# Optimization experiments

Hardware: AMD Instinct MI355X
Metric: run time of the kernel (lower is better)

Reference implementation:

```python
import jax, jax.numpy as jnp
import numpy as np

DIM = 1152
N_HEADS = 12
GROUPS = 6
KV_HEADS = N_HEADS // GROUPS  # 2
HEAD_DIM = DIM // N_HEADS     # 96
BASE = 10000.0
BSZ = 4
SEQ = 2048
MAX_SEQ = 2048
NEG_INF = -1e9


def rope(x, start_pos):
    # x: [b, s, h, d]; interleaved (even/odd) rotary embedding, matching the torch code
    b, s, h, d = x.shape
    x_even = x[..., 0::2]
    x_odd = x[..., 1::2]
    # even positions <- -x_odd, odd positions <- x_even (interleaved)
    x_rev = jnp.stack([-x_odd, x_even], axis=-1).reshape(x.shape)
    i = jnp.repeat(jnp.arange(0, d, 2), 2).astype(x.dtype)  # [d]
    theta = 1.0 / (BASE ** (i / d))                          # [d]
    pos = jnp.arange(start_pos + s, dtype=x.dtype)           # [s] (start_pos=0 case, as in source)
    ang = pos[:, None] * theta[None, :]                      # [s, d]
    cos = jnp.cos(ang).reshape(1, s, 1, d)
    sin = jnp.sin(ang).reshape(1, s, 1, d)
    return x * cos + x_rev * sin


def setup_inputs() -> dict:
    key = jax.random.key(0)
    ks = jax.random.split(key, 4)
    sc = 0.02
    x = jax.random.normal(ks[0], (BSZ, SEQ, DIM), jnp.float32)
    # causal mask [S, end_pos]: 0 on/below diagonal, large negative above
    mask = jnp.triu(jnp.full((SEQ, SEQ), NEG_INF, jnp.float32), k=1)
    q_w = jax.random.normal(ks[1], (DIM, DIM), jnp.float32) * sc
    q_b = jnp.zeros((DIM,), jnp.float32)
    kv_w = jax.random.normal(ks[2], (2 * KV_HEADS * HEAD_DIM, DIM), jnp.float32) * sc
    kv_b = jnp.zeros((2 * KV_HEADS * HEAD_DIM,), jnp.float32)
    wo_w = jax.random.normal(ks[3], (DIM, DIM), jnp.float32) * sc
    wo_b = jnp.zeros((DIM,), jnp.float32)
    return {"x": x, "mask": mask, "q_w": q_w, "q_b": q_b, "kv_w": kv_w,
            "kv_b": kv_b, "wo_w": wo_w, "wo_b": wo_b, "start_pos": 0}


def reference(x, mask, q_w, q_b, kv_w, kv_b, wo_w, wo_b, start_pos):
    b, s, f = x.shape
    end = start_pos + s
    q = (x @ q_w.T + q_b).reshape(b, s, N_HEADS, HEAD_DIM)
    kv = (x @ kv_w.T + kv_b).reshape(b, s, 2, KV_HEADS, HEAD_DIM)
    k, v = kv[:, :, 0], kv[:, :, 1]
    rq = rope(q, start_pos)
    rk = rope(k, start_pos)
    # KV-cache write (cache initialized to zeros, as in the buffer)
    k_cache = jnp.zeros((b, MAX_SEQ, KV_HEADS, HEAD_DIM), x.dtype).at[:, start_pos:end].set(rk)
    v_cache = jnp.zeros((b, MAX_SEQ, KV_HEADS, HEAD_DIM), x.dtype).at[:, start_pos:end].set(v)
    # repeat_kv: head index = kv_head * groups + g  -> jnp.repeat along head axis
    kk = jnp.repeat(k_cache[:, :end], GROUPS, axis=2)  # [b, t, H, d]
    vv = jnp.repeat(v_cache[:, :end], GROUPS, axis=2)
    scale = HEAD_DIM ** -0.5
    attn = jnp.einsum('bshd,bthd->bsht', rq, kk) * scale
    attn = attn + mask[:, None, :]  # mask [s, t] -> [s, 1, t] broadcast over b, h
    scores = jax.nn.softmax(attn.astype(jnp.float32), axis=-1).astype(x.dtype)
    out = jnp.einsum('bsht,bthd->bshd', scores, vv).reshape(b, s, DIM)
    return out @ wo_w.T + wo_b
```

## Files before the change

### kernel.cpp

```cpp
#include <hip/hip_runtime.h>
#include <hip/hip_bf16.h>

constexpr int DIMD  = 1152;
constexpr int NHD   = 12;
constexpr int KVHD  = 2;
constexpr int HDD   = 96;
constexpr int GRPS  = 6;
constexpr int SEQL  = 2048;
constexpr int BSZ4  = 4;
constexpr int MROWS = BSZ4 * SEQL;
constexpr int NQKV  = DIMD + 2 * KVHD * HDD;
constexpr float SCALE = 0.10206207261596577f;

typedef short  bf16x8 __attribute__((ext_vector_type(8)));
typedef float  f32x4  __attribute__((ext_vector_type(4)));

typedef __attribute__((address_space(3))) unsigned int       lds_u32_t;
typedef __attribute__((address_space(1))) const unsigned int glb_u32_t;

__device__ __forceinline__ void gload16(const unsigned short* g, unsigned short* l) {
    __builtin_amdgcn_global_load_lds((glb_u32_t*)(const void*)g,
                                     (lds_u32_t*)(void*)l, 16, 0, 0);
}

__device__ __forceinline__ unsigned short f2bf(float f) {
    unsigned int u = __builtin_bit_cast(unsigned int, f);
    u += 0x7fff + ((u >> 16) & 1);
    return (unsigned short)(u >> 16);
}

__device__ __forceinline__ unsigned cvtpk(float a, float b) {
    unsigned r;
    asm volatile("v_cvt_pk_bf16_f32 %0, %1, %2" : "=v"(r) : "v"(a), "v"(b));
    return r;
}

__device__ __forceinline__ void cvt4(const float4* __restrict__ s,
                                     ushort4* __restrict__ d, int i) {
    float4 f = s[i];
    ushort4 o;
    o.x = f2bf(f.x); o.y = f2bf(f.y); o.z = f2bf(f.z); o.w = f2bf(f.w);
    d[i] = o;
}

__global__ __launch_bounds__(256) void prep_kernel(
    const float4* __restrict__ x,   const float4* __restrict__ qw,
    const float4* __restrict__ kvw, const float4* __restrict__ wow,
    ushort4* __restrict__ xb,   ushort4* __restrict__ qwb,
    ushort4* __restrict__ kvwb, ushort4* __restrict__ wowb,
    const int* __restrict__ sp, float2* __restrict__ tab)
{
    constexpr int X4  = MROWS * DIMD / 4;
    constexpr int W4  = DIMD * DIMD / 4;
    constexpr int KV4 = 2 * KVHD * HDD * DIMD/4;
    constexpr int NT  = SEQL * 48;
    int i = blockIdx.x * 256 + threadIdx.x;
    if (i < X4)  { cvt4(x, xb, i); return; }
    i -= X4;
    if (i < W4)  { cvt4(qw, qwb, i); return; }
    i -= W4;
    if (i < KV4) { cvt4(kvw, kvwb, i); return; }
    i -= KV4;
    if (i < W4)  { cvt4(wow, wowb, i); return; }
    i -= W4;
    if (i < NT) {
        int s = i / 48, j = i - (i / 48) * 48;
        float th = powf(10000.0f, -(float)(2 * j) / 96.0f);
        float ang = (float)(s + *sp) * th;
        float sn, cs; sincosf(ang, &sn, &cs);
        tab[i] = make_float2(cs, sn);
    }
}

__global__ __launch_bounds__(256) void qkv_mfma_kernel(
    const unsigned short* __restrict__ xb,  const unsigned short* __restrict__ qwb,
    const unsigned short* __restrict__ kvwb,
    const float* __restrict__ qb,  const float* __restrict__ kvb,
    const float2* __restrict__ tab,
    unsigned short* __restrict__ Qo, unsigned short* __restrict__ Ko,
    unsigned short* __restrict__ VTo)
{
    __shared__ __align__(16) unsigned short As[2][128 * 32];
    __shared__ __align__(16) unsigned short Bs[2][128 * 32];

    const int tid  = threadIdx.x;
    const int w    = tid >> 6;
    const int lane = tid & 63;
    const int l16  = lane & 15;
    const int quad = lane >> 4;
    const int wm   = w >> 1, wn = w & 1;
    const int m0   = blockIdx.y * 128;
    const int n0   = blockIdx.x * 128;

    const unsigned short* Abase = xb + (size_t)m0 * DIMD;
    const unsigned short* Bbase = (n0 < DIMD)
        ? qwb  + (size_t)n0 * DIMD
        : kvwb + (size_t)(n0 - DIMD) * DIMD;

    const int srow = w * 16 + (lane >> 2);
    const int scol = (lane & 3) * 8;

    f32x4 acc[4][4];
    #pragma unroll
    for (int mi = 0; mi < 4; mi++)
        #pragma unroll
        for (int ni = 0; ni < 4; ni++) acc[mi][ni] = (f32x4){0.f, 0.f, 0.f, 0.f};

    constexpr int NK = DIMD / 32;

    gload16(Abase + (size_t)srow        * DIMD + scol, &As[0][w * 512]);
    gload16(Abase + (size_t)(srow + 64) * DIMD + scol, &As[0][2048 + w * 512]);
    gload16(Bbase + (size_t)srow        * DIMD + scol, &Bs[0][w * 512]);
    gload16(Bbase + (size_t)(srow + 64) * DIMD + scol, &Bs[0][2048 + w * 512]);

    for (int kt = 0; kt < NK; kt++) {
        const int cur = kt & 1;
        if (kt + 1 < NK) {
            const int k0 = (kt + 1) * 32;
            gload16(Abase + (size_t)srow        * DIMD + k0 + scol, &As[cur ^ 1][w * 512]);
            gload16(Abase + (size_t)(srow + 64) * DIMD + k0 + scol, &As[cur ^ 1][2048 + w * 512]);
            gload16(Bbase + (size_t)srow        * DIMD + k0 + scol, &Bs[cur ^ 1][w * 512]);
            gload16(Bbase + (size_t)(srow + 64) * DIMD + k0 + scol, &Bs[cur ^ 1][2048 + w * 512]);
            asm volatile("s_waitcnt vmcnt(4)" ::: "memory");
        } else {
            asm volatile("s_waitcnt vmcnt(0)" ::: "memory");
        }
        __builtin_amdgcn_s_barrier();
        asm volatile("" ::: "memory");

        bf16x8 af[4], bfr[4];
        #pragma unroll
        for (int mi = 0; mi < 4; mi++)
            af[mi] = *(const bf16x8*)&As[cur][(wm * 64 + mi * 16 + l16) * 32 + quad * 8];
        #pragma unroll
        for (int ni = 0; ni < 4; ni++)
            bfr[ni] = *(const bf16x8*)&Bs[cur][(wn * 64 + ni * 16 + l16) * 32 + quad * 8];
        #pragma unroll
        for (int mi = 0; mi < 4; mi++)
            #pragma unroll
            for (int ni = 0; ni < 4; ni++)
                acc[mi][ni] = __builtin_amdgcn_mfma_f32_16x16x32_bf16(
                    af[mi], bfr[ni], acc[mi][ni], 0, 0, 0);

        asm volatile("" ::: "memory");
        __builtin_amdgcn_s_barrier();
    }

    #pragma unroll
    for (int ni = 0; ni < 4; ni++) {
        const int n   = n0 + wn * 64 + ni * 16 + l16;
        const bool isQ = (n < DIMD);
        const int jj  = n - DIMD;
        const bool isK = !isQ && (jj < KVHD * HDD);
        const int d   = isQ ? (n % HDD) : (jj % HDD);
        const int hh  = isQ ? (n / HDD) : ((jj / HDD) & 1);
        const float bias = isQ ? qb[n] : kvb[jj];
        const bool doRope = isQ || isK;
        const int de2 = (d >> 1);
        const float sg = (n & 1) ? 1.0f : -1.0f;
        #pragma unroll
        for (int mi = 0; mi < 4; mi++) {
            #pragma unroll
            for (int r = 0; r < 4; r++) {
                const int m = m0 + wm * 64 + mi * 16 + quad * 4 + r;
                const int b = m >> 11;
                const int s = m & (SEQL - 1);
                float v  = acc[mi][ni][r] + bias;
                float pv = __shfl_xor(v, 1, 64);
                float o = v;
                if (doRope) {
                    float2 cs2 = tab[s * 48 + de2];
                    o = v * cs2.x + sg * pv * cs2.y;
                }
                if (isQ)
                    Qo[(((size_t)b * NHD + hh) * SEQL + s) * HDD + d] = f2bf(o);
                else if (isK)
                    Ko[(((size_t)b * KVHD + hh) * SEQL + s) * HDD + d] = f2bf(o);
                else
                    VTo[(((size_t)b * KVHD + hh) * HDD + d) * SEQL + s] = f2bf(o);
            }
        }
    }
}

__global__ __launch_bounds__(256, 3) void attn_mfma_kernel(
    const unsigned short* __restrict__ Q, const unsigned short* __restrict__ K,
    const unsigned short* __restrict__ VT, unsigned short* __restrict__ AO)
{
    constexpr int KHALF = 64 * 104;
    __shared__ __align__(16) unsigned short Ks[2 * KHALF];
    __shared__ __align__(16) unsigned short VTs[96 * 72];
    __shared__ __align__(16) unsigned short Ps[4][16 * 72];
    __shared__ float Al[4][16];

    const int tid  = threadIdx.x;
    const int w    = tid >> 6;
    const int lane = tid & 63;
    const int l16  = lane & 15;
    const int quad = lane >> 4;

    const int idx = (int)blockIdx.x;
    const int qi  = idx / 48;
    const int hb  = idx - qi * 48;
    const int qt  = 31 - qi;
    const int h   = hb % NHD;
    const int b   = hb / NHD;
    const int kvh = h / GRPS;
    const int nkb = qt + 1;

    const unsigned short* Qbase  = Q  + (((size_t)b * NHD  + h)   * SEQL) * HDD;
    const unsigned short* Kbase  = K  + (((size_t)b * KVHD + kvh) * SEQL) * HDD;
    const unsigned short* VTbase = VT + (((size_t)b * KVHD + kvh) * HDD)  * SEQL;

    int goff[7]; int gkind[7]; int loff[7];
    #pragma unroll
    for (int j = 0; j < 7; j++) {
        const int i = w + 4 * j;
        gkind[j] = 2; goff[j] = 0; loff[j] = 0;
        if (i < 13) {
            int slot = i * 64 + lane;
            int r = slot / 13, g = slot - r * 13;
            goff[j]  = r * HDD + (g < 12 ? g * 8 : 0);
            gkind[j] = 0;
            loff[j]  = i * 512;
        } else if (i < 27) {
            int iv = i - 13;
            int slot = iv * 64 + lane;
            if (slot < 864) {
                int r = slot / 9, g = slot - r * 9;
                goff[j]  = r * SEQL + (g < 8 ? g * 8 : 0);
                gkind[j] = 1;
                loff[j]  = iv * 512;
            }
        }
    }

    bf16x8 qf[3];
    {
        const int qrow = qt * 64 + w * 16 + l16;
        const unsigned short* qp = Qbase + (size_t)qrow * HDD + quad * 8;
        qf[0] = *(const bf16x8*)(qp);
        qf[1] = *(const bf16x8*)(qp + 32);
        qf[2] = *(const bf16x8*)(qp + 64);
    }

    float m_r = -1e30f, l_r = 0.0f;
    f32x4 oacc[6];
    #pragma unroll
    for (int nn = 0; nn < 6; nn++) oacc[nn] = (f32x4){0.f, 0.f, 0.f, 0.f};

    #pragma unroll
    for (int j = 0; j < 7; j++)
        if (gkind[j] == 0)
            gload16(Kbase + goff[j], &Ks[loff[j]]);
    #pragma unroll
    for (int j = 0; j < 7; j++)
        if (gkind[j] == 1) {
            if ((w + 4 * j) < 26 || lane < 32)
                gload16(VTbase + goff[j], &VTs[loff[j]]);
        }

    const int dql = w * 16 + l16;

    for (int kb = 0; kb < nkb; kb++) {
        const int  cur  = kb & 1;
        const bool more = (kb + 1 < nkb);

        if (more) {
            const size_t kg = (size_t)(kb + 1) * 64 * HDD;
            #pragma unroll
            for (int j = 0; j < 7; j++)
                if (gkind[j] == 0)
                    gload16(Kbase + kg + goff[j], &Ks[(cur ^ 1) * KHALF + loff[j]]);
            asm volatile("s_waitcnt vmcnt(6)" ::: "memory");
        } else {
            asm volatile("s_waitcnt vmcnt(3)" ::: "memory");
        }
        __builtin_amdgcn_s_barrier();
        asm volatile("" ::: "memory");

        const unsigned short* ksb = &Ks[cur * KHALF];
        f32x4 s[4];
        __builtin_amdgcn_s_setprio(1);
        #pragma unroll
        for (int n = 0; n < 4; n++) {
            const unsigned short* kr = ksb + (n * 16 + l16) * 104 + quad * 8;
            bf16x8 kf0 = *(const bf16x8*)(kr);
            bf16x8 kf1 = *(const bf16x8*)(kr + 32);
            bf16x8 kf2 = *(const bf16x8*)(kr + 64);
            f32x4 a = (f32x4){0.f, 0.f, 0.f, 0.f};
            a = __builtin_amdgcn_mfma_f32_16x16x32_bf16(kf0, qf[0], a, 0, 0, 0);
            a = __builtin_amdgcn_mfma_f32_16x16x32_bf16(kf1, qf[1], a, 0, 0, 0);
            a = __builtin_amdgcn_mfma_f32_16x16x32_bf16(kf2, qf[2], a, 0, 0, 0);
            s[n] = a;
        }
        __builtin_amdgcn_s_setprio(0);

        float v[4][4];
        float mx = -3e30f;
        if (!more) {
            #pragma unroll
            for (int n = 0; n < 4; n++)
                #pragma unroll
                for (int r = 0; r < 4; r++) {
                    float x = s[n][r] * SCALE;
                    if (n * 16 + quad * 4 + r > dql) x = -1e30f;
                    v[n][r] = x;
                    mx = fmaxf(mx, x);
                }
        } else {
            #pragma unroll
            for (int n = 0; n < 4; n++)
                #pragma unroll
                for (int r = 0; r < 4; r++) {
                    float x = s[n][r] * SCALE;
                    v[n][r] = x;
                    mx = fmaxf(mx, x);
                }
        }
        mx = fmaxf(mx, __shfl_xor(mx, 16, 64));
        mx = fmaxf(mx, __shfl_xor(mx, 32, 64));
        const float mnew = fmaxf(m_r, mx);
        const float al = __expf(m_r - mnew);
        if (quad == 0) Al[w][l16] = al;
        float sum = 0.0f;
        #pragma unroll
        for (int n = 0; n < 4; n++) {
            float p0 = __expf(v[n][0] - mnew);
            float p1 = __expf(v[n][1] - mnew);
            float p2 = __expf(v[n][2] - mnew);
            float p3 = __expf(v[n][3] - mnew);
            sum += (p0 + p1) + (p2 + p3);
            uint2 pk;
            pk.x = cvtpk(p0, p1);
            pk.y = cvtpk(p2, p3);
            *(uint2*)&Ps[w][l16 * 72 + n * 16 + quad * 4] = pk;
        }
        sum += __shfl_xor(sum, 16, 64);
        sum += __shfl_xor(sum, 32, 64);
        l_r = l_r * al + sum;
        m_r = mnew;
        __builtin_amdgcn_wave_barrier();

        const float4 alb = *(const float4*)&Al[w][quad * 4];
        bf16x8 pa0 = *(const bf16x8*)&Ps[w][l16 * 72 + quad * 8];
        bf16x8 pa1 = *(const bf16x8*)&Ps[w][l16 * 72 + 32 + quad * 8];
        const float albr[4] = {alb.x, alb.y, alb.z, alb.w};

        if (more) asm volatile("s_waitcnt vmcnt(3)" ::: "memory");
        else      asm volatile("s_waitcnt vmcnt(0)" ::: "memory");
        __builtin_amdgcn_s_barrier();
        asm volatile("" ::: "memory");

        __builtin_amdgcn_s_setprio(1);
        #pragma unroll
        for (int nn = 0; nn < 6; nn++) {
            const unsigned short* vr = &VTs[(nn * 16 + l16) * 72 + quad * 8];
            bf16x8 vb0 = *(const bf16x8*)(vr);
            bf16x8 vb1 = *(const bf16x8*)(vr + 32);
            f32x4 a = oacc[nn];
            #pragma unroll
            for (int r = 0; r < 4; r++) a[r] *= albr[r];
            a = __builtin_amdgcn_mfma_f32_16x16x32_bf16(pa0, vb0, a, 0, 0, 0);
            a = __builtin_amdgcn_mfma_f32_16x16x32_bf16(pa1, vb1, a, 0, 0, 0);
            oacc[nn] = a;
        }
        __builtin_amdgcn_s_setprio(0);

        asm volatile("" ::: "memory");
        __builtin_amdgcn_s_barrier();
        asm volatile("" ::: "memory");

        if (more) {
            const int kg = (kb + 1) * 64;
            #pragma unroll
            for (int j = 0; j < 7; j++)
                if (gkind[j] == 1) {
                    if ((w + 4 * j) < 26 || lane < 32)
                        gload16(VTbase + kg + goff[j], &VTs[loff[j]]);
                }
        }
    }

    const float linv = 1.0f / l_r;
    if (quad == 0) Al[w][l16] = linv;
    __builtin_amdgcn_wave_barrier();
    const float4 lb4 = *(const float4*)&Al[w][quad * 4];
    const float lbr[4] = {lb4.x, lb4.y, lb4.z, lb4.w};
    const int row0 = qt * 64 + w * 16 + quad * 4;
    #pragma unroll
    for (int nn = 0; nn < 6; nn++) {
        #pragma unroll
        for (int r = 0; r < 4; r++) {
            AO[((size_t)b * SEQL + row0 + r) * DIMD + h * HDD + nn * 16 + l16] =
                f2bf(oacc[nn][r] * lbr[r]);
        }
    }
}

__global__ __launch_bounds__(256) void out_mfma_kernel(
    const unsigned short* __restrict__ Ab, const unsigned short* __restrict__ Wb,
    const float* __restrict__ wob, float* __restrict__ out)
{
    __shared__ __align__(16) unsigned short As[2][128 * 32];
    __shared__ __align__(16) unsigned short Bs[2][128 * 32];

    const int tid  = threadIdx.x;
    const int w    = tid >> 6;
    const int lane = tid & 63;
    const int l16  = lane & 15;
    const int quad = lane >> 4;
    const int wm   = w >> 1, wn = w & 1;
    const int m0   = blockIdx.y * 128;
    const int n0   = blockIdx.x * 128;

    const unsigned short* Abase = Ab + (size_t)m0 * DIMD;
    const unsigned short* Bbase = Wb + (size_t)n0 * DIMD;

    const int srow = w * 16 + (lane >> 2);
    const int scol = (lane & 3) * 8;

    f32x4 acc[4][4];
    #pragma unroll
    for (int mi = 0; mi < 4; mi++)
        #pragma unroll
        for (int ni = 0; ni < 4; ni++) acc[mi][ni] = (f32x4){0.f, 0.f, 0.f, 0.f};

    constexpr int NK = DIMD / 32;

    gload16(Abase + (size_t)srow        * DIMD + scol, &As[0][w * 512]);
    gload16(Abase + (size_t)(srow + 64) * DIMD + scol, &As[0][2048 + w * 512]);
    gload16(Bbase + (size_t)srow        * DIMD + scol, &Bs[0][w * 512]);
    gload16(Bbase + (size_t)(srow + 64) * DIMD + scol, &Bs[0][2048 + w * 512]);

    for (int kt = 0; kt < NK; kt++) {
        const int cur = kt & 1;
        if (kt + 1 < NK) {
            const int k0 = (kt + 1) * 32;
            gload16(Abase + (size_t)srow        * DIMD + k0 + scol, &As[cur ^ 1][w * 512]);
            gload16(Abase + (size_t)(srow + 64) * DIMD + k0 + scol, &As[cur ^ 1][2048 + w * 512]);
            gload16(Bbase + (size_t)srow        * DIMD + k0 + scol, &Bs[cur ^ 1][w * 512]);
            gload16(Bbase + (size_t)(srow + 64) * DIMD + k0 + scol, &Bs[cur ^ 1][2048 + w * 512]);
            asm volatile("s_waitcnt vmcnt(4)" ::: "memory");
        } else {
            asm volatile("s_waitcnt vmcnt(0)" ::: "memory");
        }
        __builtin_amdgcn_s_barrier();
        asm volatile("" ::: "memory");

        bf16x8 af[4], bfr[4];
        #pragma unroll
        for (int mi = 0; mi < 4; mi++)
            af[mi] = *(const bf16x8*)&As[cur][(wm * 64 + mi * 16 + l16) * 32 + quad * 8];
        #pragma unroll
        for (int ni = 0; ni < 4; ni++)
            bfr[ni] = *(const bf16x8*)&Bs[cur][(wn * 64 + ni * 16 + l16) * 32 + quad * 8];
        #pragma unroll
        for (int mi = 0; mi < 4; mi++)
            #pragma unroll
            for (int ni = 0; ni < 4; ni++)
                acc[mi][ni] = __builtin_amdgcn_mfma_f32_16x16x32_bf16(
                    af[mi], bfr[ni], acc[mi][ni], 0, 0, 0);

        asm volatile("" ::: "memory");
        __builtin_amdgcn_s_barrier();
    }

    #pragma unroll
    for (int ni = 0; ni < 4; ni++) {
        const int n = n0 + wn * 64 + ni * 16 + l16;
        const float bias = wob[n];
        #pragma unroll
        for (int mi = 0; mi < 4; mi++) {
            #pragma unroll
            for (int r = 0; r < 4; r++) {
                const int m = m0 + wm * 64 + mi * 16 + quad * 4 + r;
                out[(size_t)m * DIMD + n] = acc[mi][ni][r] + bias;
            }
        }
    }
}

extern "C" void kernel_launch(void* const* d_in, const int* in_sizes, int n_in,
                              void* d_out, int out_size, void* d_ws, size_t ws_size,
                              hipStream_t stream)
{
    const float* x   = (const float*)d_in[0];
    const float* qw  = (const float*)d_in[2];
    const float* qb  = (const float*)d_in[3];
    const float* kvw = (const float*)d_in[4];
    const float* kvb = (const float*)d_in[5];
    const float* wow = (const float*)d_in[6];
    const float* wob = (const float*)d_in[7];
    const int*   sp  = (const int*)d_in[8];

    const size_t xN   = (size_t)MROWS * DIMD;
    const size_t qwN  = (size_t)DIMD * DIMD;
    const size_t kvwN = (size_t)2 * KVHD * HDD * DIMD;
    const size_t qN   = (size_t)BSZ4 * NHD  * SEQL * HDD;
    const size_t kvN  = (size_t)BSZ4 * KVHD * SEQL * HDD;

    unsigned short* xb   = (unsigned short*)d_ws;
    unsigned short* qwb  = xb   + xN;
    unsigned short* kvwb = qwb  + qwN;
    unsigned short* wowb = kvwb + kvwN;
    unsigned short* Q16  = wowb + qwN;
    unsigned short* K16  = Q16  + qN;
    unsigned short* VT16 = K16  + kvN;
    unsigned short* AO16 = VT16 + kvN;
    float2* tab = (float2*)AO16;

    constexpr int PREP_TOT = (MROWS * DIMD + 2 * DIMD * DIMD
                              + 2 * KVHD * HDD * DIMD) / 4 + SEQL * 48;
    prep_kernel<<<(PREP_TOT + 255) / 256, 256, 0, stream>>>(
        (const float4*)x, (const float4*)qw, (const float4*)kvw, (const float4*)wow,
        (ushort4*)xb, (ushort4*)qwb, (ushort4*)kvwb, (ushort4*)wowb, sp, tab);

    qkv_mfma_kernel<<<dim3(NQKV / 128, MROWS / 128, 1), 256, 0, stream>>>(
        xb, qwb, kvwb, qb, kvb, tab, Q16, K16, VT16);
    attn_mfma_kernel<<<dim3((SEQL / 64) * NHD * BSZ4, 1, 1), 256, 0, stream>>>(
        Q16, K16, VT16, AO16);
    out_mfma_kernel<<<dim3(DIMD / 128, MROWS / 128, 1), 256, 0, stream>>>(
        AO16, wowb, wob, (float*)d_out);
}
```

Before: 301.4 us.

## Triple-buffer LDS loads and swizzle block order in projection GEMMs

```diff
diff --git a/kernel.cpp b/kernel.cpp
--- a/kernel.cpp
+++ b/kernel.cpp
@@ -52,7 +52,7 @@
 {
     constexpr int X4  = MROWS * DIMD / 4;
     constexpr int W4  = DIMD * DIMD / 4;
-    constexpr int KV4 = 2 * KVHD * HDD * DIMD/4;
+    constexpr int KV4 = 2 * KVHD * HDD * DIMD / 4;
     constexpr int NT  = SEQL * 48;
     int i = blockIdx.x * 256 + threadIdx.x;
     if (i < X4)  { cvt4(x, xb, i); return; }
@@ -80,8 +80,8 @@
     unsigned short* __restrict__ Qo, unsigned short* __restrict__ Ko,
     unsigned short* __restrict__ VTo)
 {
-    __shared__ __align__(16) unsigned short As[2][128 * 32];
-    __shared__ __align__(16) unsigned short Bs[2][128 * 32];
+    __shared__ __align__(16) unsigned short As[3][128 * 32];
+    __shared__ __align__(16) unsigned short Bs[3][128 * 32];
 
     const int tid  = threadIdx.x;
     const int w    = tid >> 6;
@@ -89,8 +89,11 @@
     const int l16  = lane & 15;
     const int quad = lane >> 4;
     const int wm   = w >> 1, wn = w & 1;
-    const int m0   = blockIdx.y * 128;
-    const int n0   = blockIdx.x * 128;
+
+    const int flat = (int)(blockIdx.y * gridDim.x + blockIdx.x);
+    const int swz  = (flat & 7) * 96 + (flat >> 3);
+    const int m0   = (swz / 12) * 128;
+    const int n0   = (swz % 12) * 128;
 
     const unsigned short* Abase = xb + (size_t)m0 * DIMD;
     const unsigned short* Bbase = (n0 < DIMD)
@@ -112,15 +115,22 @@
     gload16(Abase + (size_t)(srow + 64) * DIMD + scol, &As[0][2048 + w * 512]);
     gload16(Bbase + (size_t)srow        * DIMD + scol, &Bs[0][w * 512]);
     gload16(Bbase + (size_t)(srow + 64) * DIMD + scol, &Bs[0][2048 + w * 512]);
+    gload16(Abase + (size_t)srow        * DIMD + 32 + scol, &As[1][w * 512]);
+    gload16(Abase + (size_t)(srow + 64) * DIMD + 32 + scol, &As[1][2048 + w * 512]);
+    gload16(Bbase + (size_t)srow        * DIMD + 32 + scol, &Bs[1][w * 512]);
+    gload16(Bbase + (size_t)(srow + 64) * DIMD + 32 + scol, &Bs[1][2048 + w * 512]);
 
     for (int kt = 0; kt < NK; kt++) {
-        const int cur = kt & 1;
-        if (kt + 1 < NK) {
-            const int k0 = (kt + 1) * 32;
-            gload16(Abase + (size_t)srow        * DIMD + k0 + scol, &As[cur ^ 1][w * 512]);
-            gload16(Abase + (size_t)(srow + 64) * DIMD + k0 + scol, &As[cur ^ 1][2048 + w * 512]);
-            gload16(Bbase + (size_t)srow        * DIMD + k0 + scol, &Bs[cur ^ 1][w * 512]);
-            gload16(Bbase + (size_t)(srow + 64) * DIMD + k0 + scol, &Bs[cur ^ 1][2048 + w * 512]);
+        const int cur = kt % 3;
+        if (kt + 2 < NK) {
+            const int stg = (kt + 2) % 3;
+            const int k0  = (kt + 2) * 32;
+            gload16(Abase + (size_t)srow        * DIMD + k0 + scol, &As[stg][w * 512]);
+            gload16(Abase + (size_t)(srow + 64) * DIMD + k0 + scol, &As[stg][2048 + w * 512]);
+            gload16(Bbase + (size_t)srow        * DIMD + k0 + scol, &Bs[stg][w * 512]);
+            gload16(Bbase + (size_t)(srow + 64) * DIMD + k0 + scol, &Bs[stg][2048 + w * 512]);
+            asm volatile("s_waitcnt vmcnt(8)" ::: "memory");
+        } else if (kt + 1 < NK) {
             asm volatile("s_waitcnt vmcnt(4)" ::: "memory");
         } else {
             asm volatile("s_waitcnt vmcnt(0)" ::: "memory");
@@ -402,8 +412,8 @@
     const unsigned short* __restrict__ Ab, const unsigned short* __restrict__ Wb,
     const float* __restrict__ wob, float* __restrict__ out)
 {
-    __shared__ __align__(16) unsigned short As[2][128 * 32];
-    __shared__ __align__(16) unsigned short Bs[2][128 * 32];
+    __shared__ __align__(16) unsigned short As[3][128 * 32];
+    __shared__ __align__(16) unsigned short Bs[3][128 * 32];
 
     const int tid  = threadIdx.x;
     const int w    = tid >> 6;
@@ -411,8 +421,11 @@
     const int l16  = lane & 15;
     const int quad = lane >> 4;
     const int wm   = w >> 1, wn = w & 1;
-    const int m0   = blockIdx.y * 128;
-    const int n0   = blockIdx.x * 128;
+
+    const int flat = (int)(blockIdx.y * gridDim.x + blockIdx.x);
+    const int swz  = (flat & 7) * 72 + (flat >> 3);
+    const int m0   = (swz / 9) * 128;
+    const int n0   = (swz % 9) * 128;
 
     const unsigned short* Abase = Ab + (size_t)m0 * DIMD;
     const unsigned short* Bbase = Wb + (size_t)n0 * DIMD;
@@ -432,15 +445,22 @@
     gload16(Abase + (size_t)(srow + 64) * DIMD + scol, &As[0][2048 + w * 512]);
     gload16(Bbase + (size_t)srow        * DIMD + scol, &Bs[0][w * 512]);
     gload16(Bbase + (size_t)(srow + 64) * DIMD + scol, &Bs[0][2048 + w * 512]);
+    gload16(Abase + (size_t)srow        * DIMD + 32 + scol, &As[1][w * 512]);
+    gload16(Abase + (size_t)(srow + 64) * DIMD + 32 + scol, &As[1][2048 + w * 512]);
+    gload16(Bbase + (size_t)srow        * DIMD + 32 + scol, &Bs[1][w * 512]);
+    gload16(Bbase + (size_t)(srow + 64) * DIMD + 32 + scol, &Bs[1][2048 + w * 512]);
 
     for (int kt = 0; kt < NK; kt++) {
-        const int cur = kt & 1;
-        if (kt + 1 < NK) {
-            const int k0 = (kt + 1) * 32;
-            gload16(Abase + (size_t)srow        * DIMD + k0 + scol, &As[cur ^ 1][w * 512]);
-            gload16(Abase + (size_t)(srow + 64) * DIMD + k0 + scol, &As[cur ^ 1][2048 + w * 512]);
-            gload16(Bbase + (size_t)srow        * DIMD + k0 + scol, &Bs[cur ^ 1][w * 512]);
-            gload16(Bbase + (size_t)(srow + 64) * DIMD + k0 + scol, &Bs[cur ^ 1][2048 + w * 512]);
+        const int cur = kt % 3;
+        if (kt + 2 < NK) {
+            const int stg = (kt + 2) % 3;
+            const int k0  = (kt + 2) * 32;
+            gload16(Abase + (size_t)srow        * DIMD + k0 + scol, &As[stg][w * 512]);
+            gload16(Abase + (size_t)(srow + 64) * DIMD + k0 + scol, &As[stg][2048 + w * 512]);
+            gload16(Bbase + (size_t)srow        * DIMD + k0 + scol, &Bs[stg][w * 512]);
+            gload16(Bbase + (size_t)(srow + 64) * DIMD + k0 + scol, &Bs[stg][2048 + w * 512]);
+            asm volatile("s_waitcnt vmcnt(8)" ::: "memory");
+        } else if (kt + 1 < NK) {
             asm volatile("s_waitcnt vmcnt(4)" ::: "memory");
         } else {
             asm volatile("s_waitcnt vmcnt(0)" ::: "memory");
```

New measurement: 288.8 us. 4.2% less time.
